# Kernel optimization log

Measured on AMD Instinct MI355X. Metric: run time of the kernel, lower is better.

## Reference

```python
import jax, jax.numpy as jnp
import numpy as np

# ---- maxflat pyramid filters (pfilters('maxflat')) ----
def _maxflat_filters():
    sqrt2 = np.sqrt(2.0)
    M1 = M2 = 1.0 / sqrt2
    k1 = 1.0 - sqrt2
    k2 = k3 = M1
    h_half = np.array([0.25 * k2 * k3, 0.5 * k2, 1.0 + 0.5 * k2 * k3]) * M1
    h = np.concatenate([h_half, h_half[:-1][::-1]]) * sqrt2          # len 5
    g_half = np.array([-0.125 * k1 * k2 * k3,
                       0.25 * k1 * k2,
                       -0.5 * k1 - 0.5 * k3 - 0.375 * k1 * k2 * k3,
                       1.0 + 0.5 * k1 * k2]) * M2
    g = np.concatenate([g_half, g_half[:-1][::-1]]) * sqrt2          # len 7
    return h.astype(np.float32), g.astype(np.float32)

# highpass from g, as in wfb2dec: h1 = -g * (-1)**(arange(1,L+1)-c)
def _wfb_filters():
    h, g = _maxflat_filters()
    len_h1 = len(g)                      # 7 (odd)
    c = int(np.floor((len_h1 + 1.0) / 2.0))   # 4
    h1 = (-g * (-1.0) ** (np.arange(1, len_h1 + 1) - c)).astype(np.float32)
    ext_h0 = int(np.floor(len(h) / 2.0))      # 2
    ext_h1 = len_h1 - c + 1                   # 4
    return h, h1, ext_h0, ext_h1

# periodic row filtering along last axis (torch rowfiltering: periodic pad +
# cross-correlation, which F.conv2d / lax conv both compute without flip)
def rowfilt(x, f, ext1):
    L = f.shape[0]
    ext2 = L - ext1 - 1
    W = x.shape[-1]
    xe = jnp.concatenate([x[..., -ext1:], x, x[..., :ext2]], axis=-1)
    y = f[0] * xe[..., 0:W]
    for k in range(1, L):                 # tiny fixed tap loop, fuses fine
        y = y + f[k] * xe[..., k:k + W]
    return y

def colfilt(x, f, ext1):
    return jnp.swapaxes(rowfilt(jnp.swapaxes(x, -1, -2), f, ext1), -1, -2)


def setup_inputs() -> dict:
    key = jax.random.key(0)
    x = jax.random.normal(key, (8, 3, 1024, 1024), dtype=jnp.float32)
    return {"x": x}


def reference(x):
    # Pycontourlet.batch_multi_channel_pdfbdec with pfilt='maxflat',
    # nlevs=[0] -> wfb2dec path: one level of separable wavelet FB with
    # periodic extension; returns [xLL, [xLH, xHL, xHH]] (stacked here).
    h_np, h1_np, e0, e1 = _wfb_filters()
    h = jnp.asarray(h_np)
    h1 = jnp.asarray(h1_np)

    x_L = rowfilt(x, h, e0)[..., ::2]          # [B,C,H,W/2]
    x_H = rowfilt(x, h1, e1)[..., ::2]

    x_LL = colfilt(x_L, h, e0)[..., ::2, :]    # [B,C,H/2,W/2]
    x_LH = colfilt(x_L, h1, e1)[..., ::2, :]
    x_HL = colfilt(x_H, h, e0)[..., ::2, :]
    x_HH = colfilt(x_H, h1, e1)[..., ::2, :]

    return jnp.stack([x_LL, x_LH, x_HL, x_HH])  # [4,B,C,H/2,W/2]
```

## Files before the change

kernel.cpp:

```cpp
#include <hip/hip_runtime.h>


constexpr int H = 1024, W = 1024;
constexpr int NIMG = 24;
constexpr int HOUT = 512, WOUT = 512;
constexpr int BROWS = 16;
constexpr int BCOLS = 64;
constexpr int TROWS = 37;
constexpr int TSEGS = 36;
constexpr int NSEG  = TROWS * TSEGS;
constexpr int NCHUNK = (NSEG + 63) / 64;
constexpr int ROWF  = TSEGS * 4;

__global__ __launch_bounds__(256)
void wfb_kernel(const float* __restrict__ x, float* __restrict__ out) {
    __shared__ __align__(16) float smem[NCHUNK * 256];

    const float h0c[5] = {0.125f, 0.35355339059327373f, 1.25f,
                          0.35355339059327373f, 0.125f};
    const float h1c[7] = {0.025888347648318447f,  0.07322330470336313f,
                          -0.06878156646177083f, -0.8535533905932737f,
                          -0.06878156646177083f,  0.07322330470336313f,
                          0.025888347648318447f};

    const int tid  = threadIdx.x;
    const int wave = tid >> 6;
    const int lane = tid & 63;
    const int img  = blockIdx.z;
    const int R0   = blockIdx.y * BROWS;
    const int J0b  = blockIdx.x * BCOLS;
    const float* __restrict__ xin = x + (size_t)img * H * W;
    const int rb0 = 2 * R0 - 4;
    const int cb0 = 2 * J0b - 4;

    for (int c = wave; c < NCHUNK; c += 4) {
        int t  = c * 64 + lane;
        int r  = t / TSEGS;
        int s  = t - r * TSEGS;
        int e  = (r >> 1) & 1;
        int gr = (rb0 + r) & (H - 1);
        int gc = (cb0 + 4 * (s ^ e)) & (W - 1);
        const float* gp = xin + ((size_t)gr << 10) + gc;
        __builtin_amdgcn_global_load_lds(
            (const __attribute__((address_space(1))) void*)gp,
            (__attribute__((address_space(3))) void*)(smem + c * 256),
            16, 0, 0);
    }
    __syncthreads();

    const int Rl = tid >> 4;
    const int s0 = (tid & 15) * 2;

    float vA[13], vB[13];
    #pragma unroll
    for (int c = 0; c < 13; ++c) { vA[c] = 0.f; vB[c] = 0.f; }

    #pragma unroll
    for (int d = 0; d < 7; ++d) {
        const int r = 2 * Rl + d;
        const int e = (r >> 1) & 1;
        const float* base = smem + r * ROWF;
        float4 f0 = *(const float4*)(base + (((s0    ) ^ e) << 2));
        float4 f1 = *(const float4*)(base + (((s0 + 1) ^ e) << 2));
        float4 f2 = *(const float4*)(base + (((s0 + 2) ^ e) << 2));
        float v12 = base[((s0 + 3) ^ e) << 2];
        float v[13] = {f0.x, f0.y, f0.z, f0.w,
                       f1.x, f1.y, f1.z, f1.w,
                       f2.x, f2.y, f2.z, f2.w, v12};
        #pragma unroll
        for (int c = 0; c < 13; ++c) vB[c] += h1c[d] * v[c];
        if (d >= 2) {
            #pragma unroll
            for (int c = 0; c < 13; ++c) vA[c] += h0c[d - 2] * v[c];
        }
    }

    float LL[4], LH[4], HL[4], HH[4];
    #pragma unroll
    for (int u = 0; u < 4; ++u) {
        const float* a = vA + 2 * u;
        const float* b = vB + 2 * u;
        LL[u] = h0c[0]*a[2] + h0c[1]*a[3] + h0c[2]*a[4]
              + h0c[3]*a[5] + h0c[4]*a[6];
        HL[u] = h1c[0]*a[0] + h1c[1]*a[1] + h1c[2]*a[2] + h1c[3]*a[3]
              + h1c[4]*a[4] + h1c[5]*a[5] + h1c[6]*a[6];
        LH[u] = h0c[0]*b[2] + h0c[1]*b[3] + h0c[2]*b[4]
              + h0c[3]*b[5] + h0c[4]*b[6];
        HH[u] = h1c[0]*b[0] + h1c[1]*b[1] + h1c[2]*b[2] + h1c[3]*b[3]
              + h1c[4]*b[4] + h1c[5]*b[5] + h1c[6]*b[6];
    }

    constexpr size_t SB = (size_t)NIMG * HOUT * WOUT;
    float* __restrict__ o = out + (size_t)img * HOUT * WOUT;
    const int R  = R0 + Rl;
    const int J0 = J0b + (tid & 15) * 4;
    const size_t off = (size_t)R * WOUT + J0;
    *(float4*)(o + 0*SB + off) = make_float4(LL[0], LL[1], LL[2], LL[3]);
    *(float4*)(o + 1*SB + off) = make_float4(LH[0], LH[1], LH[2], LH[3]);
    *(float4*)(o + 2*SB + off) = make_float4(HL[0], HL[1], HL[2], HL[3]);
    *(float4*)(o + 3*SB + off) = make_float4(HH[0], HH[1], HH[2], HH[3]);
}

extern "C" void kernel_launch(void* const* d_in, const int* in_sizes, int n_in,
                              void* d_out, int out_size, void* d_ws, size_t ws_size,
                              hipStream_t stream) {
    const float* x = (const float*)d_in[0];
    float* out = (float*)d_out;
    dim3 grid(WOUT / BCOLS, HOUT / BROWS, NIMG);
    wfb_kernel<<<grid, dim3(256), 0, stream>>>(x, out);
}
```

Baseline: 173.1 us.

## Make blocks persistent over eight row tiles with double-buffered async LDS staging

Each block now walks eight consecutive 16-row output tiles instead of one. Input tiles are staged into two LDS buffers with global_load_lds, so the next tile loads while the current one is computed, using hand-placed vmcnt waits and barriers. This hides global load latency and amortises block launch overhead. It also cuts the grid eightfold to 768 blocks, doubles LDS use per block, and depends on hard-coded vmcnt counts that must match the number of loads each wave issues.

```diff
diff --git a/kernel.cpp b/kernel.cpp
--- a/kernel.cpp
+++ b/kernel.cpp
@@ -6,15 +6,17 @@
 constexpr int HOUT = 512, WOUT = 512;
 constexpr int BROWS = 16;
 constexpr int BCOLS = 64;
+constexpr int YT    = 8;
 constexpr int TROWS = 37;
 constexpr int TSEGS = 36;
 constexpr int NSEG  = TROWS * TSEGS;
 constexpr int NCHUNK = (NSEG + 63) / 64;
 constexpr int ROWF  = TSEGS * 4;
+constexpr int BUFF  = NCHUNK * 256;
 
 __global__ __launch_bounds__(256)
 void wfb_kernel(const float* __restrict__ x, float* __restrict__ out) {
-    __shared__ __align__(16) float smem[NCHUNK * 256];
+    __shared__ __align__(16) float smem[2][BUFF];
 
     const float h0c[5] = {0.125f, 0.35355339059327373f, 1.25f,
                           0.35355339059327373f, 0.125f};
@@ -27,78 +29,97 @@
     const int wave = tid >> 6;
     const int lane = tid & 63;
     const int img  = blockIdx.z;
-    const int R0   = blockIdx.y * BROWS;
+    const int R0b  = blockIdx.y * (YT * BROWS);
     const int J0b  = blockIdx.x * BCOLS;
     const float* __restrict__ xin = x + (size_t)img * H * W;
-    const int rb0 = 2 * R0 - 4;
     const int cb0 = 2 * J0b - 4;
 
-    for (int c = wave; c < NCHUNK; c += 4) {
-        int t  = c * 64 + lane;
-        int r  = t / TSEGS;
-        int s  = t - r * TSEGS;
-        int e  = (r >> 1) & 1;
-        int gr = (rb0 + r) & (H - 1);
-        int gc = (cb0 + 4 * (s ^ e)) & (W - 1);
-        const float* gp = xin + ((size_t)gr << 10) + gc;
-        __builtin_amdgcn_global_load_lds(
-            (const __attribute__((address_space(1))) void*)gp,
-            (__attribute__((address_space(3))) void*)(smem + c * 256),
-            16, 0, 0);
-    }
-    __syncthreads();
+    auto STAGE = [&](int t, int b) {
+        const int rb0 = 2 * (R0b + t * BROWS) - 4;
+        for (int c = wave; c < NCHUNK; c += 4) {
+            int u  = c * 64 + lane;
+            int r  = u / TSEGS;
+            int s  = u - r * TSEGS;
+            int e  = (r >> 1) & 1;
+            int gr = (rb0 + r) & (H - 1);
+            int gc = (cb0 + 4 * (s ^ e)) & (W - 1);
+            const float* gp = xin + ((size_t)gr << 10) + gc;
+            __builtin_amdgcn_global_load_lds(
+                (const __attribute__((address_space(1))) void*)gp,
+                (__attribute__((address_space(3))) void*)(&smem[b][c * 256]),
+                16, 0, 0);
+        }
+    };
 
     const int Rl = tid >> 4;
     const int s0 = (tid & 15) * 2;
+    constexpr size_t SB = (size_t)NIMG * HOUT * WOUT;
+    float* __restrict__ o = out + (size_t)img * HOUT * WOUT;
 
-    float vA[13], vB[13];
-    #pragma unroll
-    for (int c = 0; c < 13; ++c) { vA[c] = 0.f; vB[c] = 0.f; }
+    STAGE(0, 0);
+    STAGE(1, 1);
 
     #pragma unroll
-    for (int d = 0; d < 7; ++d) {
-        const int r = 2 * Rl + d;
-        const int e = (r >> 1) & 1;
-        const float* base = smem + r * ROWF;
-        float4 f0 = *(const float4*)(base + (((s0    ) ^ e) << 2));
-        float4 f1 = *(const float4*)(base + (((s0 + 1) ^ e) << 2));
-        float4 f2 = *(const float4*)(base + (((s0 + 2) ^ e) << 2));
-        float v12 = base[((s0 + 3) ^ e) << 2];
-        float v[13] = {f0.x, f0.y, f0.z, f0.w,
-                       f1.x, f1.y, f1.z, f1.w,
-                       f2.x, f2.y, f2.z, f2.w, v12};
+    for (int t = 0; t < YT; ++t) {
+        if (t == 0)           asm volatile("s_waitcnt vmcnt(5)" ::: "memory");
+        else if (t == YT - 1) asm volatile("s_waitcnt vmcnt(4)" ::: "memory");
+        else                  asm volatile("s_waitcnt vmcnt(9)" ::: "memory");
+        __builtin_amdgcn_s_barrier();
+        __builtin_amdgcn_sched_barrier(0);
+
+        const float* __restrict__ bufc = smem[t & 1];
+        float vA[13], vB[13];
         #pragma unroll
-        for (int c = 0; c < 13; ++c) vB[c] += h1c[d] * v[c];
-        if (d >= 2) {
+        for (int c = 0; c < 13; ++c) { vA[c] = 0.f; vB[c] = 0.f; }
+
+        #pragma unroll
+        for (int d = 0; d < 7; ++d) {
+            const int r = 2 * Rl + d;
+            const int e = (r >> 1) & 1;
+            const float* base = bufc + r * ROWF;
+            float4 f0 = *(const float4*)(base + (((s0    ) ^ e) << 2));
+            float4 f1 = *(const float4*)(base + (((s0 + 1) ^ e) << 2));
+            float4 f2 = *(const float4*)(base + (((s0 + 2) ^ e) << 2));
+            float v12 = base[((s0 + 3) ^ e) << 2];
+            float v[13] = {f0.x, f0.y, f0.z, f0.w,
+                           f1.x, f1.y, f1.z, f1.w,
+                           f2.x, f2.y, f2.z, f2.w, v12};
             #pragma unroll
-            for (int c = 0; c < 13; ++c) vA[c] += h0c[d - 2] * v[c];
+            for (int c = 0; c < 13; ++c) vB[c] += h1c[d] * v[c];
+            if (d >= 2) {
+                #pragma unroll
+                for (int c = 0; c < 13; ++c) vA[c] += h0c[d - 2] * v[c];
+            }
         }
+
+        __builtin_amdgcn_sched_barrier(0);
+        __builtin_amdgcn_s_barrier();
+        __builtin_amdgcn_sched_barrier(0);
+        if (t + 2 < YT) STAGE(t + 2, t & 1);
+        __builtin_amdgcn_sched_barrier(0);
+
+        float LL[4], LH[4], HL[4], HH[4];
+        #pragma unroll
+        for (int u = 0; u < 4; ++u) {
+            const float* a = vA + 2 * u;
+            const float* b = vB + 2 * u;
+            LL[u] = h0c[0]*a[2] + h0c[1]*a[3] + h0c[2]*a[4]
+                  + h0c[3]*a[5] + h0c[4]*a[6];
+            HL[u] = h1c[0]*a[0] + h1c[1]*a[1] + h1c[2]*a[2] + h1c[3]*a[3]
+                  + h1c[4]*a[4] + h1c[5]*a[5] + h1c[6]*a[6];
+            LH[u] = h0c[0]*b[2] + h0c[1]*b[3] + h0c[2]*b[4]
+                  + h0c[3]*b[5] + h0c[4]*b[6];
+            HH[u] = h1c[0]*b[0] + h1c[1]*b[1] + h1c[2]*b[2] + h1c[3]*b[3]
+                  + h1c[4]*b[4] + h1c[5]*b[5] + h1c[6]*b[6];
+        }
+        const int R  = R0b + t * BROWS + Rl;
+        const int J0 = J0b + (tid & 15) * 4;
+        const size_t off = (size_t)R * WOUT + J0;
+        *(float4*)(o + 0*SB + off) = make_float4(LL[0], LL[1], LL[2], LL[3]);
+        *(float4*)(o + 1*SB + off) = make_float4(LH[0], LH[1], LH[2], LH[3]);
+        *(float4*)(o + 2*SB + off) = make_float4(HL[0], HL[1], HL[2], HL[3]);
+        *(float4*)(o + 3*SB + off) = make_float4(HH[0], HH[1], HH[2], HH[3]);
     }
-
-    float LL[4], LH[4], HL[4], HH[4];
-    #pragma unroll
-    for (int u = 0; u < 4; ++u) {
-        const float* a = vA + 2 * u;
-        const float* b = vB + 2 * u;
-        LL[u] = h0c[0]*a[2] + h0c[1]*a[3] + h0c[2]*a[4]
-              + h0c[3]*a[5] + h0c[4]*a[6];
-        HL[u] = h1c[0]*a[0] + h1c[1]*a[1] + h1c[2]*a[2] + h1c[3]*a[3]
-              + h1c[4]*a[4] + h1c[5]*a[5] + h1c[6]*a[6];
-        LH[u] = h0c[0]*b[2] + h0c[1]*b[3] + h0c[2]*b[4]
-              + h0c[3]*b[5] + h0c[4]*b[6];
-        HH[u] = h1c[0]*b[0] + h1c[1]*b[1] + h1c[2]*b[2] + h1c[3]*b[3]
-              + h1c[4]*b[4] + h1c[5]*b[5] + h1c[6]*b[6];
-    }
-
-    constexpr size_t SB = (size_t)NIMG * HOUT * WOUT;
-    float* __restrict__ o = out + (size_t)img * HOUT * WOUT;
-    const int R  = R0 + Rl;
-    const int J0 = J0b + (tid & 15) * 4;
-    const size_t off = (size_t)R * WOUT + J0;
-    *(float4*)(o + 0*SB + off) = make_float4(LL[0], LL[1], LL[2], LL[3]);
-    *(float4*)(o + 1*SB + off) = make_float4(LH[0], LH[1], LH[2], LH[3]);
-    *(float4*)(o + 2*SB + off) = make_float4(HL[0], HL[1], HL[2], HL[3]);
-    *(float4*)(o + 3*SB + off) = make_float4(HH[0], HH[1], HH[2], HH[3]);
 }
 
 extern "C" void kernel_launch(void* const* d_in, const int* in_sizes, int n_in,
@@ -106,6 +127,6 @@
                               hipStream_t stream) {
     const float* x = (const float*)d_in[0];
     float* out = (float*)d_out;
-    dim3 grid(WOUT / BCOLS, HOUT / BROWS, NIMG);
+    dim3 grid(WOUT / BCOLS, HOUT / (BROWS * YT), NIMG);
     wfb_kernel<<<grid, dim3(256), 0, stream>>>(x, out);
 }
```

Measured after the change: 180.7 us. 4.4% more time.
